# Performance work log

Measured on AMD Instinct MI355X. Metric: run time of the kernel, lower is better.

## Reference

```python
import jax, jax.numpy as jnp
from jax import lax
import numpy as np

EPS = 1e-6
DN = ('NCHW', 'OIHW', 'NCHW')  # conv dimension numbers matching torch F.conv2d


def setup_inputs() -> dict:
    key = jax.random.key(0)
    kx, ky = jax.random.split(key)
    B, C, H, W = 16, 3, 512, 512
    x = jax.random.normal(kx, (B, C, H, W), dtype=jnp.float32)
    y = jax.random.normal(ky, (B, C, H, W), dtype=jnp.float32)
    return {"x": x, "y": y}


def _box_smooth(v):
    # 7x7 uniform kernel repeated over 3 input channels -> 1 output channel,
    # every tap weighted 1/49 (matches kernel.repeat(1,3,1,1) in torch).
    k = jnp.full((1, v.shape[1], 7, 7), 1.0 / 49.0, dtype=v.dtype)
    return lax.conv_general_dilated(v, k, window_strides=(1, 1),
                                    padding=[(3, 3), (3, 3)],
                                    dimension_numbers=DN)


def reference(x, y):
    # conv is linear, so conv(x) - conv(y) == conv(x - y); avoids one conv pass
    diff = _box_smooth(x - y)           # [B, 1, H, W]
    return jnp.mean(jnp.sqrt(diff * diff + EPS))  # scalar Charbonnier loss
```

## Files before the change

### kernel.cpp

```cpp
#include <hip/hip_runtime.h>
#include <math.h>


namespace {
constexpr int kB = 16, kC = 3, kH = 512, kW = 512;
constexpr int TH = 32;
constexpr int TW = 64;
constexpr int RH = TH + 6;
constexpr int RW = TW + 8;
constexpr int RW4 = RW / 4;
constexpr int SLOTS = RH * RW4;
constexpr int NT = 256;
constexpr int K = 3;
constexpr int NTILES = (kW / TW) * (kH / TH) * kB;
constexpr int NBLOCKS = 512;
constexpr int TPB = NTILES / NBLOCKS;
}

__global__ __launch_bounds__(NT, 4)
void charbox_kernel(const float* __restrict__ x, const float* __restrict__ y,
                    float* __restrict__ out) {
  __shared__ float zs[RH][RW];
  __shared__ float red[NT / 64];

  const int tid = threadIdx.x;
  const size_t HW = (size_t)kH * kW;

  int rr[K], cc[K];
  bool ex[K];
#pragma unroll
  for (int k = 0; k < K; ++k) {
    const int s = tid + k * NT;
    rr[k] = s / RW4;
    cc[k] = (s - rr[k] * RW4) * 4;
    ex[k] = (s < SLOTS);
  }

  float4 xr[K][3], yr[K][3];
  bool img[K];

  auto issue = [&](int id) {
    const int tx = id & 7, ty = (id >> 3) & 15, b = id >> 7;
    const int w0 = tx * TW, h0 = ty * TH;
    const float* xb = x + (size_t)b * kC * HW;
    const float* yb = y + (size_t)b * kC * HW;
#pragma unroll
    for (int k = 0; k < K; ++k) {
      const int h  = h0 - 3 + rr[k];
      const int wb = w0 - 4 + cc[k];
      img[k] = ex[k] & ((unsigned)h < (unsigned)kH) & ((unsigned)wb < (unsigned)kW);
      const int hc = min(max(h, 0), kH - 1);
      const int wc = min(max(wb, 0), kW - 4);
      const float* px = xb + (size_t)hc * kW + wc;
      const float* py = yb + (size_t)hc * kW + wc;
      xr[k][0] = *(const float4*)px;
      xr[k][1] = *(const float4*)(px + HW);
      xr[k][2] = *(const float4*)(px + 2 * HW);
      yr[k][0] = *(const float4*)py;
      yr[k][1] = *(const float4*)(py + HW);
      yr[k][2] = *(const float4*)(py + 2 * HW);
    }
  };

  float acc = 0.f;
  const int wi = tid & 63;
  const int g  = tid >> 6;
  const int r0 = g * 8;

  issue(blockIdx.x);

  for (int it = 0; it < TPB; ++it) {
#pragma unroll
    for (int k = 0; k < K; ++k) {
      if (ex[k]) {
        float4 z = make_float4(0.f, 0.f, 0.f, 0.f);
        if (img[k]) {
          z.x = (xr[k][0].x - yr[k][0].x) + (xr[k][1].x - yr[k][1].x) + (xr[k][2].x - yr[k][2].x);
          z.y = (xr[k][0].y - yr[k][0].y) + (xr[k][1].y - yr[k][1].y) + (xr[k][2].y - yr[k][2].y);
          z.z = (xr[k][0].z - yr[k][0].z) + (xr[k][1].z - yr[k][1].z) + (xr[k][2].z - yr[k][2].z);
          z.w = (xr[k][0].w - yr[k][0].w) + (xr[k][1].w - yr[k][1].w) + (xr[k][2].w - yr[k][2].w);
        }
        *(float4*)&zs[rr[k]][cc[k]] = z;
      }
    }
    __syncthreads();

    if (it + 1 < TPB) issue((it + 1) * NBLOCKS + blockIdx.x);

    float hbuf[7];
    float v = 0.f;
#pragma unroll
    for (int k = 0; k < 7; ++k) {
      const float* zr = &zs[r0 + k][wi + 1];
      const float a = ((zr[0] + zr[1]) + (zr[2] + zr[3])) + ((zr[4] + zr[5]) + zr[6]);
      hbuf[k] = a;
      v += a;
    }
    {
      const float d = v * (1.0f / 49.0f);
      acc += sqrtf(fmaf(d, d, 1e-6f));
    }
#pragma unroll
    for (int k = 0; k < 7; ++k) {
      const float* zr = &zs[r0 + 7 + k][wi + 1];
      const float hn = ((zr[0] + zr[1]) + (zr[2] + zr[3])) + ((zr[4] + zr[5]) + zr[6]);
      v += hn - hbuf[k];
      const float d = v * (1.0f / 49.0f);
      acc += sqrtf(fmaf(d, d, 1e-6f));
    }
    __syncthreads();
  }

#pragma unroll
  for (int off = 32; off > 0; off >>= 1) acc += __shfl_down(acc, off, 64);
  if (wi == 0) red[g] = acc;
  __syncthreads();
  if (tid == 0) {
    const float ssum = red[0] + red[1] + red[2] + red[3];
    atomicAdd(out, ssum * (1.0f / ((float)kB * (float)kH * (float)kW)));
  }
}

extern "C" void kernel_launch(void* const* d_in, const int* in_sizes, int n_in,
                              void* d_out, int out_size, void* d_ws, size_t ws_size,
                              hipStream_t stream) {
  const float* x = (const float*)d_in[0];
  const float* y = (const float*)d_in[1];
  float* out = (float*)d_out;

  charbox_kernel<<<NBLOCKS, NT, 0, stream>>>(x, y, out);
}
```

Measured before the change: 123.8 us.

## Replace shared-memory tiles with per-wave row bands using shuffles and register rings

Each wavefront now owns an 8-row band across the full 512-pixel width, with each lane holding 8 columns. Horizontal box sums use lane shuffles for halo columns and vertical sums use a 7-row register ring buffer with running sums. Rows are double-buffered in registers. This removes shared memory, block barriers and redundant halo loads within a row. In exchange, each band rereads 6 halo rows (about 75% extra vertical traffic versus 8 rows), there are only 2 waves per block, and register pressure is high.

```diff
diff --git a/kernel.cpp b/kernel.cpp
--- a/kernel.cpp
+++ b/kernel.cpp
@@ -4,119 +4,136 @@
 
 namespace {
 constexpr int kB = 16, kC = 3, kH = 512, kW = 512;
-constexpr int TH = 32;
-constexpr int TW = 64;
-constexpr int RH = TH + 6;
-constexpr int RW = TW + 8;
-constexpr int RW4 = RW / 4;
-constexpr int SLOTS = RH * RW4;
-constexpr int NT = 256;
-constexpr int K = 3;
-constexpr int NTILES = (kW / TW) * (kH / TH) * kB;
-constexpr int NBLOCKS = 512;
-constexpr int TPB = NTILES / NBLOCKS;
+constexpr int ROWS = 8;
+constexpr int BANDS_PER_IMG = kH / ROWS;
+constexpr int NBANDS = kB * BANDS_PER_IMG;
+constexpr int WPB = 2;
+constexpr int NT = WPB * 64;
+constexpr int NB = NBANDS / WPB;
+constexpr float EPS = 1e-6f;
 }
 
-__global__ __launch_bounds__(NT, 4)
+struct RowRegs { float4 a[6]; float4 b[6]; };
+
+__device__ __forceinline__ void issue_row(RowRegs& R,
+                                          const float* __restrict__ xb,
+                                          const float* __restrict__ yb,
+                                          int rclamp, int c0) {
+  const size_t HW = (size_t)kH * kW;
+  const float* px = xb + (size_t)rclamp * kW + c0;
+  const float* py = yb + (size_t)rclamp * kW + c0;
+#pragma unroll
+  for (int ch = 0; ch < 3; ++ch) {
+    R.a[ch]     = *(const float4*)(px + ch * HW);
+    R.b[ch]     = *(const float4*)(px + ch * HW + 4);
+    R.a[3 + ch] = *(const float4*)(py + ch * HW);
+    R.b[3 + ch] = *(const float4*)(py + ch * HW + 4);
+  }
+}
+
+__global__ __launch_bounds__(NT, 1)
 void charbox_kernel(const float* __restrict__ x, const float* __restrict__ y,
                     float* __restrict__ out) {
-  __shared__ float zs[RH][RW];
-  __shared__ float red[NT / 64];
+  __shared__ float red[WPB];
 
-  const int tid = threadIdx.x;
+  const int tid  = threadIdx.x;
+  const int lane = tid & 63;
+  const int wid  = tid >> 6;
+  const int band = blockIdx.x * WPB + wid;
+  const int b    = band >> 6;
+  const int r0   = (band & 63) * ROWS;
   const size_t HW = (size_t)kH * kW;
+  const float* xb = x + (size_t)b * kC * HW;
+  const float* yb = y + (size_t)b * kC * HW;
+  const int c0 = lane * 8;
+  const int laneL = (lane + 63) & 63;
+  const int laneR = (lane + 1) & 63;
 
-  int rr[K], cc[K];
-  bool ex[K];
+  float ring[7][8];
+  float v[8];
 #pragma unroll
-  for (int k = 0; k < K; ++k) {
-    const int s = tid + k * NT;
-    rr[k] = s / RW4;
-    cc[k] = (s - rr[k] * RW4) * 4;
-    ex[k] = (s < SLOTS);
-  }
+  for (int k = 0; k < 7; ++k)
+#pragma unroll
+    for (int j = 0; j < 8; ++j) ring[k][j] = 0.f;
+#pragma unroll
+  for (int j = 0; j < 8; ++j) v[j] = 0.f;
+  float acc = 0.f;
 
-  float4 xr[K][3], yr[K][3];
-  bool img[K];
+  RowRegs buf[2];
+  issue_row(buf[0], xb, yb, max(r0 - 3, 0), c0);
 
-  auto issue = [&](int id) {
-    const int tx = id & 7, ty = (id >> 3) & 15, b = id >> 7;
-    const int w0 = tx * TW, h0 = ty * TH;
-    const float* xb = x + (size_t)b * kC * HW;
-    const float* yb = y + (size_t)b * kC * HW;
 #pragma unroll
-    for (int k = 0; k < K; ++k) {
-      const int h  = h0 - 3 + rr[k];
-      const int wb = w0 - 4 + cc[k];
-      img[k] = ex[k] & ((unsigned)h < (unsigned)kH) & ((unsigned)wb < (unsigned)kW);
-      const int hc = min(max(h, 0), kH - 1);
-      const int wc = min(max(wb, 0), kW - 4);
-      const float* px = xb + (size_t)hc * kW + wc;
-      const float* py = yb + (size_t)hc * kW + wc;
-      xr[k][0] = *(const float4*)px;
-      xr[k][1] = *(const float4*)(px + HW);
-      xr[k][2] = *(const float4*)(px + 2 * HW);
-      yr[k][0] = *(const float4*)py;
-      yr[k][1] = *(const float4*)(py + HW);
-      yr[k][2] = *(const float4*)(py + 2 * HW);
+  for (int it = 0; it < ROWS + 6; ++it) {
+    if (it + 1 < ROWS + 6) {
+      const int rn = r0 - 3 + it + 1;
+      issue_row(buf[(it + 1) & 1], xb, yb, min(max(rn, 0), kH - 1), c0);
     }
-  };
+    const RowRegs& R = buf[it & 1];
+    const int r = r0 - 3 + it;
+    const bool valid = (r >= 0) & (r < kH);
 
-  float acc = 0.f;
-  const int wi = tid & 63;
-  const int g  = tid >> 6;
-  const int r0 = g * 8;
+    float z[8];
+    if (valid) {
+      z[0] = (R.a[0].x - R.a[3].x) + (R.a[1].x - R.a[4].x) + (R.a[2].x - R.a[5].x);
+      z[1] = (R.a[0].y - R.a[3].y) + (R.a[1].y - R.a[4].y) + (R.a[2].y - R.a[5].y);
+      z[2] = (R.a[0].z - R.a[3].z) + (R.a[1].z - R.a[4].z) + (R.a[2].z - R.a[5].z);
+      z[3] = (R.a[0].w - R.a[3].w) + (R.a[1].w - R.a[4].w) + (R.a[2].w - R.a[5].w);
+      z[4] = (R.b[0].x - R.b[3].x) + (R.b[1].x - R.b[4].x) + (R.b[2].x - R.b[5].x);
+      z[5] = (R.b[0].y - R.b[3].y) + (R.b[1].y - R.b[4].y) + (R.b[2].y - R.b[5].y);
+      z[6] = (R.b[0].z - R.b[3].z) + (R.b[1].z - R.b[4].z) + (R.b[2].z - R.b[5].z);
+      z[7] = (R.b[0].w - R.b[3].w) + (R.b[1].w - R.b[4].w) + (R.b[2].w - R.b[5].w);
+    } else {
+#pragma unroll
+      for (int j = 0; j < 8; ++j) z[j] = 0.f;
+    }
 
-  issue(blockIdx.x);
+    const float l5 = __shfl(z[5], laneL, 64);
+    const float l6 = __shfl(z[6], laneL, 64);
+    const float l7 = __shfl(z[7], laneL, 64);
+    const float g0 = __shfl(z[0], laneR, 64);
+    const float g1 = __shfl(z[1], laneR, 64);
+    const float g2 = __shfl(z[2], laneR, 64);
+    float e[14];
+    e[0] = lane ? l5 : 0.f;
+    e[1] = lane ? l6 : 0.f;
+    e[2] = lane ? l7 : 0.f;
+#pragma unroll
+    for (int j = 0; j < 8; ++j) e[3 + j] = z[j];
+    e[11] = (lane < 63) ? g0 : 0.f;
+    e[12] = (lane < 63) ? g1 : 0.f;
+    e[13] = (lane < 63) ? g2 : 0.f;
 
-  for (int it = 0; it < TPB; ++it) {
+    float h[8];
+    float s = ((e[0] + e[1]) + (e[2] + e[3])) + ((e[4] + e[5]) + e[6]);
+    h[0] = s;
 #pragma unroll
-    for (int k = 0; k < K; ++k) {
-      if (ex[k]) {
-        float4 z = make_float4(0.f, 0.f, 0.f, 0.f);
-        if (img[k]) {
-          z.x = (xr[k][0].x - yr[k][0].x) + (xr[k][1].x - yr[k][1].x) + (xr[k][2].x - yr[k][2].x);
-          z.y = (xr[k][0].y - yr[k][0].y) + (xr[k][1].y - yr[k][1].y) + (xr[k][2].y - yr[k][2].y);
-          z.z = (xr[k][0].z - yr[k][0].z) + (xr[k][1].z - yr[k][1].z) + (xr[k][2].z - yr[k][2].z);
-          z.w = (xr[k][0].w - yr[k][0].w) + (xr[k][1].w - yr[k][1].w) + (xr[k][2].w - yr[k][2].w);
-        }
-        *(float4*)&zs[rr[k]][cc[k]] = z;
+    for (int j = 1; j < 8; ++j) {
+      s += e[j + 6] - e[j - 1];
+      h[j] = s;
+    }
+
+    const int slot = it % 7;
+#pragma unroll
+    for (int j = 0; j < 8; ++j) {
+      v[j] += h[j] - ring[slot][j];
+      ring[slot][j] = h[j];
+    }
+
+    if (it >= 6) {
+#pragma unroll
+      for (int j = 0; j < 8; ++j) {
+        const float d = v[j] * (1.0f / 49.0f);
+        acc += sqrtf(fmaf(d, d, EPS));
       }
     }
-    __syncthreads();
-
-    if (it + 1 < TPB) issue((it + 1) * NBLOCKS + blockIdx.x);
-
-    float hbuf[7];
-    float v = 0.f;
-#pragma unroll
-    for (int k = 0; k < 7; ++k) {
-      const float* zr = &zs[r0 + k][wi + 1];
-      const float a = ((zr[0] + zr[1]) + (zr[2] + zr[3])) + ((zr[4] + zr[5]) + zr[6]);
-      hbuf[k] = a;
-      v += a;
-    }
-    {
-      const float d = v * (1.0f / 49.0f);
-      acc += sqrtf(fmaf(d, d, 1e-6f));
-    }
-#pragma unroll
-    for (int k = 0; k < 7; ++k) {
-      const float* zr = &zs[r0 + 7 + k][wi + 1];
-      const float hn = ((zr[0] + zr[1]) + (zr[2] + zr[3])) + ((zr[4] + zr[5]) + zr[6]);
-      v += hn - hbuf[k];
-      const float d = v * (1.0f / 49.0f);
-      acc += sqrtf(fmaf(d, d, 1e-6f));
-    }
-    __syncthreads();
   }
 
 #pragma unroll
   for (int off = 32; off > 0; off >>= 1) acc += __shfl_down(acc, off, 64);
-  if (wi == 0) red[g] = acc;
+  if (lane == 0) red[wid] = acc;
   __syncthreads();
   if (tid == 0) {
-    const float ssum = red[0] + red[1] + red[2] + red[3];
+    const float ssum = red[0] + red[1];
     atomicAdd(out, ssum * (1.0f / ((float)kB * (float)kH * (float)kW)));
   }
 }
@@ -128,5 +145,5 @@
   const float* y = (const float*)d_in[1];
   float* out = (float*)d_out;
 
-  charbox_kernel<<<NBLOCKS, NT, 0, stream>>>(x, y, out);
+  charbox_kernel<<<NB, NT, 0, stream>>>(x, y, out);
 }
```

New measurement: 126.2 us. No clear change (+1.9%).
